# Kernel optimization log

Measured on AMD Instinct MI355X. Metric: run time of the kernel, lower is better.

The kernel has to match this reference:

```python
import jax, jax.numpy as jnp
import numpy as np


def setup_inputs() -> dict:
    key = jax.random.key(0)
    ks = jax.random.split(key, 6)
    B, H, T, Dk, Dv = 64, 16, 4, 128, 256
    q = jax.random.normal(ks[0], (B, H, T, Dk), dtype=jnp.float32)
    k = jax.random.normal(ks[1], (B, H, T, Dk), dtype=jnp.float32)
    v = jax.random.normal(ks[2], (B, H, T, Dv), dtype=jnp.float32)
    g = jax.random.uniform(ks[3], (B, H, T), dtype=jnp.float32)
    beta = jax.random.uniform(ks[4], (B, H, T), dtype=jnp.float32)
    last_recurrent_state = jax.random.normal(ks[5], (B, H, Dk, Dv), dtype=jnp.float32)
    return {"q": q, "k": k, "v": v, "g": g, "beta": beta,
            "last_recurrent_state": last_recurrent_state}


def reference(q, k, v, g, beta, last_recurrent_state):
    # q,k: (B,H,T,Dk)  v: (B,H,T,Dv)  g,beta: (B,H,T)  state: (B,H,Dk,Dv)
    def step(state, xs):
        q_t, k_t, v_t, g_t, beta_t = xs  # (B,H,Dk),(B,H,Dk),(B,H,Dv),(B,H),(B,H)
        state = state * jnp.exp(g_t)[..., None, None]           # decay
        kv_mem = jnp.einsum('bhkv,bhk->bhv', state, k_t)         # readout with key
        delta = (v_t - kv_mem) * beta_t[..., None]               # delta-rule correction
        state = state + k_t[..., None] * delta[..., None, :]     # rank-1 update
        out_t = jnp.einsum('bhkv,bhk->bhv', state, q_t)          # query readout
        return state, out_t

    xs = (jnp.moveaxis(q, 2, 0), jnp.moveaxis(k, 2, 0), jnp.moveaxis(v, 2, 0),
          jnp.moveaxis(g, 2, 0), jnp.moveaxis(beta, 2, 0))
    state, outs = jax.lax.scan(step, last_recurrent_state, xs)
    output = jnp.moveaxis(outs, 0, 2)  # (B,H,T,Dv)
    return jnp.concatenate([output.reshape(-1), state.reshape(-1)], axis=0)
```

## Files before the change

### kernel.cpp

```cpp
#include <hip/hip_runtime.h>

#define BH    1024
#define TT    4
#define DK    128
#define DV    256
#define KSEG  8
#define KLEN  16
#define HALFV 128
#define LDP   17

__global__ __launch_bounds__(256)
void delta_rule_kernel(const float* __restrict__ q,
                       const float* __restrict__ k,
                       const float* __restrict__ v,
                       const float* __restrict__ g,
                       const float* __restrict__ beta,
                       const float* __restrict__ s0,
                       float* __restrict__ out)
{
    const int bh   = blockIdx.x >> 1;
    const int half = blockIdx.x & 1;
    const int tid  = threadIdx.x;
    const int kg   = tid & (KSEG - 1);
    const int vg   = tid >> 3;
    const int vcol = half * HALFV + vg * 4;
    const int kr0  = kg * KLEN;

    const float* __restrict__ sin_p = s0 + (size_t)bh * DK * DV;
    float* __restrict__ out_p  = out + (size_t)bh * TT * DV;
    float* __restrict__ sout_p = out + (size_t)BH * TT * DV + (size_t)bh * DK * DV;

    const float* __restrict__ kbase = k    + (size_t)bh * TT * DK;
    const float* __restrict__ qbase = q    + (size_t)bh * TT * DK;
    const float* __restrict__ vbase = v    + (size_t)bh * TT * DV;
    const float* __restrict__ gbase = g    + (size_t)bh * TT;
    const float* __restrict__ bbase = beta + (size_t)bh * TT;

    float4 s4[KLEN];
#pragma unroll
    for (int kk = 0; kk < KLEN; ++kk)
        s4[kk] = *(const float4*)&sin_p[(size_t)(kr0 + kk) * DV + vcol];

    __shared__ float ks[KSEG * LDP];
    __shared__ float qs[KSEG * LDP];

    for (int t = 0; t < TT; ++t) {
        __syncthreads();
        if (tid < DK) {
            ks[(tid >> 4) * LDP + (tid & 15)] = kbase[t * DK + tid];
        } else {
            int j = tid - DK;
            qs[(j >> 4) * LDP + (j & 15)] = qbase[t * DK + j];
        }
        __syncthreads();

        const float gt = expf(gbase[t]);
        const float bt = bbase[t];
        const float4 v4 = *(const float4*)&vbase[t * DV + vcol];

        float4 kv = make_float4(0.f, 0.f, 0.f, 0.f);
#pragma unroll
        for (int kk = 0; kk < KLEN; ++kk) {
            const float kt = ks[kg * LDP + kk];
            s4[kk].x *= gt; s4[kk].y *= gt; s4[kk].z *= gt; s4[kk].w *= gt;
            kv.x = fmaf(s4[kk].x, kt, kv.x);
            kv.y = fmaf(s4[kk].y, kt, kv.y);
            kv.z = fmaf(s4[kk].z, kt, kv.z);
            kv.w = fmaf(s4[kk].w, kt, kv.w);
        }
#pragma unroll
        for (int m = 1; m < KSEG; m <<= 1) {
            kv.x += __shfl_xor(kv.x, m);
            kv.y += __shfl_xor(kv.y, m);
            kv.z += __shfl_xor(kv.z, m);
            kv.w += __shfl_xor(kv.w, m);
        }

        float4 d4;
        d4.x = (v4.x - kv.x) * bt;
        d4.y = (v4.y - kv.y) * bt;
        d4.z = (v4.z - kv.z) * bt;
        d4.w = (v4.w - kv.w) * bt;

        float4 o4 = make_float4(0.f, 0.f, 0.f, 0.f);
#pragma unroll
        for (int kk = 0; kk < KLEN; ++kk) {
            const float kt = ks[kg * LDP + kk];
            const float qt = qs[kg * LDP + kk];
            s4[kk].x = fmaf(kt, d4.x, s4[kk].x);
            s4[kk].y = fmaf(kt, d4.y, s4[kk].y);
            s4[kk].z = fmaf(kt, d4.z, s4[kk].z);
            s4[kk].w = fmaf(kt, d4.w, s4[kk].w);
            o4.x = fmaf(s4[kk].x, qt, o4.x);
            o4.y = fmaf(s4[kk].y, qt, o4.y);
            o4.z = fmaf(s4[kk].z, qt, o4.z);
            o4.w = fmaf(s4[kk].w, qt, o4.w);
        }
#pragma unroll
        for (int m = 1; m < KSEG; m <<= 1) {
            o4.x += __shfl_xor(o4.x, m);
            o4.y += __shfl_xor(o4.y, m);
            o4.z += __shfl_xor(o4.z, m);
            o4.w += __shfl_xor(o4.w, m);
        }
        if (kg == 0)
            *(float4*)&out_p[t * DV + vcol] = o4;
    }

#pragma unroll
    for (int kk = 0; kk < KLEN; ++kk)
        *(float4*)&sout_p[(size_t)(kr0 + kk) * DV + vcol] = s4[kk];
}

extern "C" void kernel_launch(void* const* d_in, const int* in_sizes, int n_in,
                              void* d_out, int out_size, void* d_ws, size_t ws_size,
                              hipStream_t stream) {
    const float* q    = (const float*)d_in[0];
    const float* k    = (const float*)d_in[1];
    const float* v    = (const float*)d_in[2];
    const float* g    = (const float*)d_in[3];
    const float* beta = (const float*)d_in[4];
    const float* s0   = (const float*)d_in[5];
    float* out = (float*)d_out;

    delta_rule_kernel<<<dim3(BH * 2), dim3(256), 0, stream>>>(q, k, v, g, beta, s0, out);
}
```

Before: 262.3 us.

## Reformulate four-step delta rule as chunked form with one state pass

Replaces the sequential per-timestep scan with a chunked algebraic form. The kernel computes all four k·S0 and q·S0 projections against the initial state, plus the small k·k and k·q Gram matrices via wavefront shuffles. It then solves the delta corrections with a triangular recurrence and writes the final state in a single pass using cumulative decay products. The goal is fewer state passes, fewer block-wide syncs and less per-step reduction overhead. In exchange it adds many cross-lane shuffle reductions and changes the floating-point summation order.

```diff
diff --git a/kernel.cpp b/kernel.cpp
--- a/kernel.cpp
+++ b/kernel.cpp
@@ -1,13 +1,12 @@
 #include <hip/hip_runtime.h>
 
-#define BH    1024
-#define TT    4
-#define DK    128
-#define DV    256
-#define KSEG  8
-#define KLEN  16
-#define HALFV 128
-#define LDP   17
+#define BH 1024
+#define TT 4
+#define DK 128
+#define DV 256
+#define NW 4
+#define RPW 32
+#define CH 128
 
 __global__ __launch_bounds__(256)
 void delta_rule_kernel(const float* __restrict__ q,
@@ -21,10 +20,11 @@
     const int bh   = blockIdx.x >> 1;
     const int half = blockIdx.x & 1;
     const int tid  = threadIdx.x;
-    const int kg   = tid & (KSEG - 1);
-    const int vg   = tid >> 3;
-    const int vcol = half * HALFV + vg * 4;
-    const int kr0  = kg * KLEN;
+    const int w    = tid >> 6;
+    const int l    = tid & 63;
+    const int col  = half * CH + (l << 1);
+    const int lc   = l << 1;
+    const int r0   = w * RPW;
 
     const float* __restrict__ sin_p = s0 + (size_t)bh * DK * DV;
     float* __restrict__ out_p  = out + (size_t)bh * TT * DV;
@@ -36,80 +36,155 @@
     const float* __restrict__ gbase = g    + (size_t)bh * TT;
     const float* __restrict__ bbase = beta + (size_t)bh * TT;
 
-    float4 s4[KLEN];
-#pragma unroll
-    for (int kk = 0; kk < KLEN; ++kk)
-        s4[kk] = *(const float4*)&sin_p[(size_t)(kr0 + kk) * DV + vcol];
-
-    __shared__ float ks[KSEG * LDP];
-    __shared__ float qs[KSEG * LDP];
-
+    __shared__ __align__(16) float ksh[DK][4];
+    __shared__ __align__(16) float qsh[DK][4];
+    __shared__ __align__(16) float red[TT][NW][CH];
+
+    const int e0 = tid, e1 = tid + 256;
+    const float kl0 = kbase[e0], kl1 = kbase[e1];
+    const float ql0 = qbase[e0], ql1 = qbase[e1];
+
+    const float4 gq = *(const float4*)&gbase[0];
+    const float4 bq = *(const float4*)&bbase[0];
+    float2 va[TT];
+#pragma unroll
+    for (int t = 0; t < TT; ++t)
+        va[t] = *(const float2*)&vbase[t * DV + col];
+
+    float2 s2[RPW];
+#pragma unroll
+    for (int i = 0; i < RPW; ++i)
+        s2[i] = *(const float2*)&sin_p[(size_t)(r0 + i) * DV + col];
+
+    ksh[e0 & 127][e0 >> 7] = kl0;
+    ksh[e1 & 127][e1 >> 7] = kl1;
+    qsh[e0 & 127][e0 >> 7] = ql0;
+    qsh[e1 & 127][e1 >> 7] = ql1;
+    __syncthreads();
+
+    const float y0 = expf(gq.x), y1 = expf(gq.y), y2 = expf(gq.z), y3 = expf(gq.w);
+    const float G0 = y0, G1 = y0*y1, G2 = y0*y1*y2, G3 = y0*y1*y2*y3;
+    const float M01 = y1, M02 = y1*y2, M03 = y1*y2*y3;
+    const float M12 = y2, M13 = y2*y3;
+    const float M23 = y3;
+    const float E = G3;
+    const float bt0 = bq.x, bt1 = bq.y, bt2 = bq.z, bt3 = bq.w;
+
+    const float4 kA = *(const float4*)&ksh[l][0];
+    const float4 kB = *(const float4*)&ksh[l + 64][0];
+    const float4 qA = *(const float4*)&qsh[l][0];
+    const float4 qB = *(const float4*)&qsh[l + 64][0];
+    const float a0[4] = {kA.x, kA.y, kA.z, kA.w};
+    const float a1[4] = {kB.x, kB.y, kB.z, kB.w};
+    const float b0[4] = {qA.x, qA.y, qA.z, qA.w};
+    const float b1[4] = {qB.x, qB.y, qB.z, qB.w};
+    float AA[4][4];
+    float BB[4][4];
+#pragma unroll
+    for (int s = 0; s < 4; ++s) {
+#pragma unroll
+        for (int t = 0; t < 4; ++t) {
+            if (t > s) {
+                float x = fmaf(a1[s], a1[t], a0[s] * a0[t]);
+#pragma unroll
+                for (int m = 1; m < 64; m <<= 1) x += __shfl_xor(x, m);
+                AA[s][t] = x;
+            }
+            if (t >= s) {
+                float x = fmaf(a1[s], b1[t], a0[s] * b0[t]);
+#pragma unroll
+                for (int m = 1; m < 64; m <<= 1) x += __shfl_xor(x, m);
+                BB[s][t] = x;
+            }
+        }
+    }
+
+    float2 c[TT] = {{0.f,0.f},{0.f,0.f},{0.f,0.f},{0.f,0.f}};
+#pragma unroll
+    for (int i = 0; i < RPW; ++i) {
+        const float4 k4 = *(const float4*)&ksh[r0 + i][0];
+        c[0].x = fmaf(s2[i].x, k4.x, c[0].x); c[0].y = fmaf(s2[i].y, k4.x, c[0].y);
+        c[1].x = fmaf(s2[i].x, k4.y, c[1].x); c[1].y = fmaf(s2[i].y, k4.y, c[1].y);
+        c[2].x = fmaf(s2[i].x, k4.z, c[2].x); c[2].y = fmaf(s2[i].y, k4.z, c[2].y);
+        c[3].x = fmaf(s2[i].x, k4.w, c[3].x); c[3].y = fmaf(s2[i].y, k4.w, c[3].y);
+    }
+#pragma unroll
+    for (int t = 0; t < TT; ++t)
+        *(float2*)&red[t][w][lc] = c[t];
+    __syncthreads();
+#pragma unroll
     for (int t = 0; t < TT; ++t) {
-        __syncthreads();
-        if (tid < DK) {
-            ks[(tid >> 4) * LDP + (tid & 15)] = kbase[t * DK + tid];
-        } else {
-            int j = tid - DK;
-            qs[(j >> 4) * LDP + (j & 15)] = qbase[t * DK + j];
+        const float2 u0 = *(const float2*)&red[t][0][lc];
+        const float2 u1 = *(const float2*)&red[t][1][lc];
+        const float2 u2 = *(const float2*)&red[t][2][lc];
+        const float2 u3 = *(const float2*)&red[t][3][lc];
+        c[t].x = (u0.x + u1.x) + (u2.x + u3.x);
+        c[t].y = (u0.y + u1.y) + (u2.y + u3.y);
+    }
+
+    float2 d0, d1, d2, d3;
+    d0.x = bt0 * (va[0].x - G0 * c[0].x);
+    d0.y = bt0 * (va[0].y - G0 * c[0].y);
+    d1.x = bt1 * (va[1].x - G1 * c[1].x - M01 * AA[0][1] * d0.x);
+    d1.y = bt1 * (va[1].y - G1 * c[1].y - M01 * AA[0][1] * d0.y);
+    d2.x = bt2 * (va[2].x - G2 * c[2].x - M02 * AA[0][2] * d0.x - M12 * AA[1][2] * d1.x);
+    d2.y = bt2 * (va[2].y - G2 * c[2].y - M02 * AA[0][2] * d0.y - M12 * AA[1][2] * d1.y);
+    d3.x = bt3 * (va[3].x - G3 * c[3].x - M03 * AA[0][3] * d0.x - M13 * AA[1][3] * d1.x - M23 * AA[2][3] * d2.x);
+    d3.y = bt3 * (va[3].y - G3 * c[3].y - M03 * AA[0][3] * d0.y - M13 * AA[1][3] * d1.y - M23 * AA[2][3] * d2.y);
+
+    const float W0t = M03, W1t = M13, W2t = M23;
+    float2 p[TT] = {{0.f,0.f},{0.f,0.f},{0.f,0.f},{0.f,0.f}};
+#pragma unroll
+    for (int i = 0; i < RPW; ++i) {
+        const int r = r0 + i;
+        const float4 k4 = *(const float4*)&ksh[r][0];
+        const float4 q4 = *(const float4*)&qsh[r][0];
+        const float2 s = s2[i];
+        p[0].x = fmaf(s.x, q4.x, p[0].x); p[0].y = fmaf(s.y, q4.x, p[0].y);
+        p[1].x = fmaf(s.x, q4.y, p[1].x); p[1].y = fmaf(s.y, q4.y, p[1].y);
+        p[2].x = fmaf(s.x, q4.z, p[2].x); p[2].y = fmaf(s.y, q4.z, p[2].y);
+        p[3].x = fmaf(s.x, q4.w, p[3].x); p[3].y = fmaf(s.y, q4.w, p[3].y);
+        const float h0 = W0t * k4.x, h1 = W1t * k4.y, h2 = W2t * k4.z, h3 = k4.w;
+        float nx = s.x * E, ny = s.y * E;
+        nx = fmaf(h0, d0.x, nx); ny = fmaf(h0, d0.y, ny);
+        nx = fmaf(h1, d1.x, nx); ny = fmaf(h1, d1.y, ny);
+        nx = fmaf(h2, d2.x, nx); ny = fmaf(h2, d2.y, ny);
+        nx = fmaf(h3, d3.x, nx); ny = fmaf(h3, d3.y, ny);
+        *(float2*)&sout_p[(size_t)r * DV + col] = make_float2(nx, ny);
+    }
+
+    __syncthreads();
+#pragma unroll
+    for (int t = 0; t < TT; ++t)
+        *(float2*)&red[t][w][lc] = p[t];
+    __syncthreads();
+
+    const float2 darr[4] = {d0, d1, d2, d3};
+    const float Gt[4] = {G0, G1, G2, G3};
+    const float Mm[4][4] = {{1.f, M01, M02, M03},
+                            {0.f, 1.f, M12, M13},
+                            {0.f, 0.f, 1.f, M23},
+                            {0.f, 0.f, 0.f, 1.f}};
+#pragma unroll
+    for (int t = 0; t < TT; ++t) {
+        if (w == t) {
+            const float2 u0 = *(const float2*)&red[t][0][lc];
+            const float2 u1 = *(const float2*)&red[t][1][lc];
+            const float2 u2 = *(const float2*)&red[t][2][lc];
+            const float2 u3 = *(const float2*)&red[t][3][lc];
+            float ox = Gt[t] * ((u0.x + u1.x) + (u2.x + u3.x));
+            float oy = Gt[t] * ((u0.y + u1.y) + (u2.y + u3.y));
+#pragma unroll
+            for (int s = 0; s < TT; ++s) {
+                if (s <= t) {
+                    const float cf = Mm[s][t] * BB[s][t];
+                    ox = fmaf(cf, darr[s].x, ox);
+                    oy = fmaf(cf, darr[s].y, oy);
+                }
+            }
+            *(float2*)&out_p[t * DV + col] = make_float2(ox, oy);
         }
-        __syncthreads();
-
-        const float gt = expf(gbase[t]);
-        const float bt = bbase[t];
-        const float4 v4 = *(const float4*)&vbase[t * DV + vcol];
-
-        float4 kv = make_float4(0.f, 0.f, 0.f, 0.f);
-#pragma unroll
-        for (int kk = 0; kk < KLEN; ++kk) {
-            const float kt = ks[kg * LDP + kk];
-            s4[kk].x *= gt; s4[kk].y *= gt; s4[kk].z *= gt; s4[kk].w *= gt;
-            kv.x = fmaf(s4[kk].x, kt, kv.x);
-            kv.y = fmaf(s4[kk].y, kt, kv.y);
-            kv.z = fmaf(s4[kk].z, kt, kv.z);
-            kv.w = fmaf(s4[kk].w, kt, kv.w);
-        }
-#pragma unroll
-        for (int m = 1; m < KSEG; m <<= 1) {
-            kv.x += __shfl_xor(kv.x, m);
-            kv.y += __shfl_xor(kv.y, m);
-            kv.z += __shfl_xor(kv.z, m);
-            kv.w += __shfl_xor(kv.w, m);
-        }
-
-        float4 d4;
-        d4.x = (v4.x - kv.x) * bt;
-        d4.y = (v4.y - kv.y) * bt;
-        d4.z = (v4.z - kv.z) * bt;
-        d4.w = (v4.w - kv.w) * bt;
-
-        float4 o4 = make_float4(0.f, 0.f, 0.f, 0.f);
-#pragma unroll
-        for (int kk = 0; kk < KLEN; ++kk) {
-            const float kt = ks[kg * LDP + kk];
-            const float qt = qs[kg * LDP + kk];
-            s4[kk].x = fmaf(kt, d4.x, s4[kk].x);
-            s4[kk].y = fmaf(kt, d4.y, s4[kk].y);
-            s4[kk].z = fmaf(kt, d4.z, s4[kk].z);
-            s4[kk].w = fmaf(kt, d4.w, s4[kk].w);
-            o4.x = fmaf(s4[kk].x, qt, o4.x);
-            o4.y = fmaf(s4[kk].y, qt, o4.y);
-            o4.z = fmaf(s4[kk].z, qt, o4.z);
-            o4.w = fmaf(s4[kk].w, qt, o4.w);
-        }
-#pragma unroll
-        for (int m = 1; m < KSEG; m <<= 1) {
-            o4.x += __shfl_xor(o4.x, m);
-            o4.y += __shfl_xor(o4.y, m);
-            o4.z += __shfl_xor(o4.z, m);
-            o4.w += __shfl_xor(o4.w, m);
-        }
-        if (kg == 0)
-            *(float4*)&out_p[t * DV + vcol] = o4;
-    }
-
-#pragma unroll
-    for (int kk = 0; kk < KLEN; ++kk)
-        *(float4*)&sout_p[(size_t)(kr0 + kk) * DV + vcol] = s4[kk];
+    }
 }
 
 extern "C" void kernel_launch(void* const* d_in, const int* in_sizes, int n_in,
```

Result: faster. 248.6 us (-5.2%).
